# Kernel tuning notes

Measured on AMD Instinct MI355X. Metric: run time of the kernel, lower is better.

The kernel has to match this reference:

```python
import jax, jax.numpy as jnp
import numpy as np

N = 100000
E = 1600000
EPS = 1e-16
NEG_SLOPE = 0.2


def setup_inputs() -> dict:
    key = jax.random.key(0)
    ks = jax.random.split(key, 10)
    F_in, C = 512, 40
    H1, D1 = 8, 8
    return {
        "x": jax.random.normal(ks[0], (N, F_in), jnp.float32),
        "edge_index": jax.random.randint(ks[1], (2, E), 0, N, jnp.int64),
        "W1": jax.random.normal(ks[2], (F_in, H1 * D1), jnp.float32) * 0.05,
        "att_src1": jax.random.normal(ks[3], (H1, D1), jnp.float32) * 0.1,
        "att_dst1": jax.random.normal(ks[4], (H1, D1), jnp.float32) * 0.1,
        "b1": jnp.zeros((H1 * D1,), jnp.float32),
        "W2": jax.random.normal(ks[5], (H1 * D1, C), jnp.float32) * 0.05,
        "att_src2": jax.random.normal(ks[6], (1, C), jnp.float32) * 0.1,
        "att_dst2": jax.random.normal(ks[7], (1, C), jnp.float32) * 0.1,
        "b2": jnp.zeros((C,), jnp.float32),
    }


def gat_conv(x, W, att_src, att_dst, bias, src, dst, heads, out_dim, concat):
    # Linear transform per head: [N, H, D]
    h = (x @ W).reshape(N, heads, out_dim)
    # Per-node attention logits: [N, H]
    a_src = jnp.einsum("nhd,hd->nh", h, att_src)
    a_dst = jnp.einsum("nhd,hd->nh", h, att_dst)
    # Per-edge logits (edge j->i: src=j, softmax grouped by dst=i)
    e = a_src[src] + a_dst[dst]                      # [E', H]
    e = jax.nn.leaky_relu(e, NEG_SLOPE)
    # Segment softmax over destination nodes (numerically stable)
    m = jax.ops.segment_max(e, dst, num_segments=N)  # [N, H]
    e = jnp.exp(e - m[dst])
    s = jax.ops.segment_sum(e, dst, num_segments=N)  # [N, H]
    alpha = e / (s[dst] + EPS)                       # [E', H]
    # Weighted message aggregation (scatter-add)
    msg = h[src] * alpha[:, :, None]                 # [E', H, D]
    out = jax.ops.segment_sum(msg, dst, num_segments=N)  # [N, H, D]
    out = out.reshape(N, heads * out_dim) if concat else out.mean(axis=1)
    return out + bias


def reference(x, edge_index, W1, att_src1, att_dst1, b1, W2, att_src2, att_dst2, b2):
    # PyG GATConv default: add self-loops
    loops = jnp.arange(N, dtype=edge_index.dtype)
    src = jnp.concatenate([edge_index[0], loops])
    dst = jnp.concatenate([edge_index[1], loops])
    h = gat_conv(x, W1, att_src1, att_dst1, b1, src, dst, heads=8, out_dim=8, concat=True)
    h = jax.nn.elu(h)
    out = gat_conv(h, W2, att_src2, att_dst2, b2, src, dst, heads=1, out_dim=40, concat=False)
    return jax.nn.log_softmax(out, axis=1)
```

## Files before the change

kernel.cpp:

```cpp
#include <hip/hip_runtime.h>
#include <cstdint>

#define N_NODES 100000
#define N_EDGES 1600000
#define ETOT    1700000
#define FIN     512
#define HD1     64
#define NB      80
#define C2      40
#define NEG_SLOPE 0.2f
#define SCAN_NB ((N_NODES + 1023) / 1024)

typedef __attribute__((ext_vector_type(8))) short bf16x8;
typedef __attribute__((ext_vector_type(4))) float f32x4;

__device__ __forceinline__ float lrelu(float v) { return v > 0.f ? v : NEG_SLOPE * v; }

__device__ __forceinline__ unsigned short f2bf(float f) {
    uint32_t u = __float_as_uint(f);
    u += 0x7FFF + ((u >> 16) & 1);
    return (unsigned short)(u >> 16);
}
__device__ __forceinline__ float bf2f(unsigned short u) {
    return __uint_as_float(((uint32_t)u) << 16);
}

__global__ void k_prep(const float* __restrict__ W1, const float* __restrict__ a_s,
                       const float* __restrict__ a_d,
                       const float* __restrict__ W2, const float* __restrict__ att_s2,
                       const float* __restrict__ att_d2,
                       unsigned short* __restrict__ W1t, unsigned short* __restrict__ W2t) {
    if (blockIdx.x < 160) {
        int t = blockIdx.x * 256 + threadIdx.x;
        int n = t >> 9, k = t & 511;
        float v;
        if (n < 64) {
            v = W1[k * HD1 + n];
        } else if (n < 72) {
            int h = n - 64; v = 0.f;
#pragma unroll
            for (int d = 0; d < 8; d++) v += W1[k * HD1 + h * 8 + d] * a_s[h * 8 + d];
        } else {
            int h = n - 72; v = 0.f;
#pragma unroll
            for (int d = 0; d < 8; d++) v += W1[k * HD1 + h * 8 + d] * a_d[h * 8 + d];
        }
        W1t[n * FIN + k] = f2bf(v);
    } else {
        int t = (blockIdx.x - 160) * 256 + threadIdx.x;
        if (t >= 48 * 64) return;
        int n = t >> 6, k = t & 63;
        float v = 0.f;
        if (n < C2) {
            v = W2[k * C2 + n];
        } else if (n == C2) {
            for (int c = 0; c < C2; c++) v += W2[k * C2 + c] * att_s2[c];
        } else if (n == C2 + 1) {
            for (int c = 0; c < C2; c++) v += W2[k * C2 + c] * att_d2[c];
        }
        W2t[n * 64 + k] = f2bf(v);
    }
}

__global__ __launch_bounds__(256) void k_gemm1(const float* __restrict__ x,
                                               const unsigned short* __restrict__ W1t,
                                               unsigned short* __restrict__ h1b,
                                               float* __restrict__ as1,
                                               float* __restrict__ ad1) {
    __shared__ unsigned short As[128 * 72];
    const int t    = threadIdx.x;
    const int lane = t & 63, wv = t >> 6;
    const int quad = lane >> 4, l16 = lane & 15;
    const int row0 = blockIdx.x * 128;

    f32x4 acc[2][5];
#pragma unroll
    for (int mi = 0; mi < 2; mi++)
#pragma unroll
        for (int ni = 0; ni < 5; ni++) acc[mi][ni] = (f32x4){0.f, 0.f, 0.f, 0.f};

    float4 rx[8];
#pragma unroll
    for (int i = 0; i < 8; i++) {
        int ff = t + i * 256;
        int r = ff >> 4, c4 = ff & 15;
        int row = row0 + r;
        rx[i] = (row < N_NODES) ? *(const float4*)&x[(size_t)row * FIN + c4 * 4]
                                : make_float4(0.f, 0.f, 0.f, 0.f);
    }

    for (int c = 0; c < 8; c++) {
#pragma unroll
        for (int i = 0; i < 8; i++) {
            int ff = t + i * 256;
            int r = ff >> 4, c4 = ff & 15;
            ushort4 s4;
            s4.x = f2bf(rx[i].x); s4.y = f2bf(rx[i].y);
            s4.z = f2bf(rx[i].z); s4.w = f2bf(rx[i].w);
            *(ushort4*)&As[r * 72 + c4 * 4] = s4;
        }
        __syncthreads();
        if (c < 7) {
            int kb = (c + 1) * 64;
#pragma unroll
            for (int i = 0; i < 8; i++) {
                int ff = t + i * 256;
                int r = ff >> 4, c4 = ff & 15;
                int row = row0 + r;
                rx[i] = (row < N_NODES) ? *(const float4*)&x[(size_t)row * FIN + kb + c4 * 4]
                                        : make_float4(0.f, 0.f, 0.f, 0.f);
            }
        }
        int kb = c * 64;
#pragma unroll
        for (int ks = 0; ks < 2; ks++) {
            bf16x8 af[2], bfv[5];
#pragma unroll
            for (int mi = 0; mi < 2; mi++) {
                int lr = wv * 32 + mi * 16 + l16;
                af[mi] = *(const bf16x8*)&As[lr * 72 + ks * 32 + quad * 8];
            }
#pragma unroll
            for (int ni = 0; ni < 5; ni++) {
                int n = ni * 16 + l16;
                bfv[ni] = *(const bf16x8*)&W1t[n * FIN + kb + ks * 32 + quad * 8];
            }
#pragma unroll
            for (int mi = 0; mi < 2; mi++)
#pragma unroll
                for (int ni = 0; ni < 5; ni++)
                    acc[mi][ni] = __builtin_amdgcn_mfma_f32_16x16x32_bf16(
                        af[mi], bfv[ni], acc[mi][ni], 0, 0, 0);
        }
        __syncthreads();
    }
#pragma unroll
    for (int mi = 0; mi < 2; mi++)
#pragma unroll
        for (int ni = 0; ni < 5; ni++)
#pragma unroll
            for (int r = 0; r < 4; r++) {
                int row = row0 + wv * 32 + mi * 16 + quad * 4 + r;
                if (row >= N_NODES) continue;
                int col = ni * 16 + l16;
                float v = acc[mi][ni][r];
                if (col < 64)       h1b[(size_t)row * 64 + col] = f2bf(v);
                else if (col < 72)  as1[row * 8 + (col - 64)] = v;
                else                ad1[row * 8 + (col - 72)] = v;
            }
}

__global__ void k_deg(const int* __restrict__ ei, int* __restrict__ deg) {
    int e = blockIdx.x * 256 + threadIdx.x;
    if (e >= ETOT) return;
    int dst = (e < N_EDGES) ? ei[N_EDGES + e] : e - N_EDGES;
    atomicAdd(&deg[dst], 1);
}

__global__ __launch_bounds__(1024) void k_bsum(const int* __restrict__ deg,
                                               int* __restrict__ bsum) {
    __shared__ int wsm[16];
    int t = threadIdx.x;
    int i = blockIdx.x * 1024 + t;
    int v = (i < N_NODES) ? deg[i] : 0;
#pragma unroll
    for (int o = 32; o >= 1; o >>= 1) v += __shfl_xor(v, o, 64);
    if ((t & 63) == 0) wsm[t >> 6] = v;
    __syncthreads();
    if (t < 16) {
        int s = wsm[t];
#pragma unroll
        for (int o = 8; o >= 1; o >>= 1) s += __shfl_xor(s, o, 16);
        if (t == 0) bsum[blockIdx.x] = s;
    }
}

__global__ __launch_bounds__(128) void k_bscan(const int* __restrict__ bsum,
                                               int* __restrict__ boff) {
    __shared__ int sh[128];
    int t = threadIdx.x;
    int v = (t < SCAN_NB) ? bsum[t] : 0;
    sh[t] = v;
    __syncthreads();
    for (int off = 1; off < 128; off <<= 1) {
        int u = (t >= off) ? sh[t - off] : 0;
        __syncthreads();
        sh[t] += u;
        __syncthreads();
    }
    boff[t] = sh[t] - v;
}

__global__ __launch_bounds__(1024) void k_scan3(const int* __restrict__ deg,
                                                const int* __restrict__ boff,
                                                int* __restrict__ row_ptr) {
    __shared__ int sh[1024];
    int t = threadIdx.x;
    int i = blockIdx.x * 1024 + t;
    int v = (i < N_NODES) ? deg[i] : 0;
    sh[t] = v;
    __syncthreads();
    for (int off = 1; off < 1024; off <<= 1) {
        int u = (t >= off) ? sh[t - off] : 0;
        __syncthreads();
        sh[t] += u;
        __syncthreads();
    }
    int base = boff[blockIdx.x];
    if (i < N_NODES) row_ptr[i] = base + sh[t] - v;
    if (i == N_NODES - 1) row_ptr[N_NODES] = base + sh[t];
}

__global__ void k_scatter(const int* __restrict__ ei, const int* __restrict__ row_ptr,
                          int* __restrict__ cnt, int* __restrict__ csr_src) {
    int e = blockIdx.x * 256 + threadIdx.x;
    if (e >= ETOT) return;
    int src, dst;
    if (e < N_EDGES) { src = ei[e]; dst = ei[N_EDGES + e]; }
    else             { src = dst = e - N_EDGES; }
    int pos = row_ptr[dst] + atomicAdd(&cnt[dst], 1);
    csr_src[pos] = src;
}

__global__ __launch_bounds__(256) void k_agg1(
    const unsigned short* __restrict__ h1b,
    const float* __restrict__ as1, const float* __restrict__ ad1,
    const int* __restrict__ row_ptr, const int* __restrict__ csr_src,
    const float* __restrict__ b1, unsigned short* __restrict__ hb) {
    int t = threadIdx.x, wv = t >> 6, lane = t & 63;
    int dst = blockIdx.x * 4 + wv;
    if (dst >= N_NODES) return;
    int h = lane >> 3;
    int s0 = row_ptr[dst], s1e = row_ptr[dst + 1];
    float adh = ad1[dst * 8 + h];
    float acc = 0.f, den = 0.f;
    for (int base = s0; base < s1e; base += 64) {
        int idx = base + lane;
        int sl = (idx < s1e) ? csr_src[idx] : 0;
        int cnt = min(64, s1e - base);
        int j = 0;
        for (; j + 4 <= cnt; j += 4) {
#pragma unroll
            for (int jj = 0; jj < 4; jj++) {
                int s = __shfl(sl, j + jj);
                float w = __expf(lrelu(as1[s * 8 + h] + adh));
                den += w;
                acc += w * bf2f(h1b[(size_t)s * 64 + lane]);
            }
        }
        for (; j < cnt; j++) {
            int s = __shfl(sl, j);
            float w = __expf(lrelu(as1[s * 8 + h] + adh));
            den += w;
            acc += w * bf2f(h1b[(size_t)s * 64 + lane]);
        }
    }
    float hv = acc / (den + 1e-16f) + b1[lane];
    hv = hv > 0.f ? hv : expm1f(hv);
    hb[(size_t)dst * 64 + lane] = f2bf(hv);
}

__global__ __launch_bounds__(256) void k_gemm2(const unsigned short* __restrict__ hb,
                                               const unsigned short* __restrict__ W2t,
                                               unsigned short* __restrict__ h2b,
                                               float* __restrict__ as2,
                                               float* __restrict__ ad2) {
    const int t = threadIdx.x;
    const int lane = t & 63, wv = t >> 6;
    const int quad = lane >> 4, l16 = lane & 15;
    const int row0 = blockIdx.x * 128;

    f32x4 acc[2][3];
#pragma unroll
    for (int mi = 0; mi < 2; mi++)
#pragma unroll
        for (int ni = 0; ni < 3; ni++) acc[mi][ni] = (f32x4){0.f, 0.f, 0.f, 0.f};

    bf16x8 bfrag[2][3];
#pragma unroll
    for (int ks = 0; ks < 2; ks++)
#pragma unroll
        for (int ni = 0; ni < 3; ni++)
            bfrag[ks][ni] = *(const bf16x8*)&W2t[(ni * 16 + l16) * 64 + ks * 32 + quad * 8];

#pragma unroll
    for (int mi = 0; mi < 2; mi++) {
        int row = row0 + wv * 32 + mi * 16 + l16;
        int rowc = row < N_NODES ? row : N_NODES - 1;
#pragma unroll
        for (int ks = 0; ks < 2; ks++) {
            bf16x8 af = *(const bf16x8*)&hb[(size_t)rowc * 64 + ks * 32 + quad * 8];
#pragma unroll
            for (int ni = 0; ni < 3; ni++)
                acc[mi][ni] = __builtin_amdgcn_mfma_f32_16x16x32_bf16(
                    af, bfrag[ks][ni], acc[mi][ni], 0, 0, 0);
        }
    }
#pragma unroll
    for (int mi = 0; mi < 2; mi++)
#pragma unroll
        for (int ni = 0; ni < 3; ni++)
#pragma unroll
            for (int r = 0; r < 4; r++) {
                int row = row0 + wv * 32 + mi * 16 + quad * 4 + r;
                if (row >= N_NODES) continue;
                int col = ni * 16 + l16;
                float v = acc[mi][ni][r];
                if (col < C2)            h2b[(size_t)row * C2 + col] = f2bf(v);
                else if (col == C2)      as2[row] = v;
                else if (col == C2 + 1)  ad2[row] = v;
            }
}

__global__ __launch_bounds__(256) void k_agg2(
    const unsigned short* __restrict__ h2b,
    const float* __restrict__ as2, const float* __restrict__ ad2,
    const int* __restrict__ row_ptr, const int* __restrict__ csr_src,
    const float* __restrict__ b2, float* __restrict__ out) {
    int t = threadIdx.x, wv = t >> 6, lane = t & 63;
    int dst = blockIdx.x * 4 + wv;
    if (dst >= N_NODES) return;
    int s0 = row_ptr[dst], s1e = row_ptr[dst + 1];
    float ad = ad2[dst];
    bool act = lane < C2;
    int cl = act ? lane : 0;
    float acc = 0.f, den = 0.f;
    for (int base = s0; base < s1e; base += 64) {
        int idx = base + lane;
        bool vld = idx < s1e;
        int sl = vld ? csr_src[idx] : 0;
        float wl = vld ? __expf(lrelu(as2[sl] + ad)) : 0.f;
        float d = wl;
#pragma unroll
        for (int o = 32; o >= 1; o >>= 1) d += __shfl_xor(d, o, 64);
        den += d;
        int cnt  = min(64, s1e - base);
        int cnt4 = (cnt + 3) & ~3;
        for (int j = 0; j < cnt4; j += 4) {
#pragma unroll
            for (int jj = 0; jj < 4; jj++) {
                int s   = __shfl(sl, j + jj);
                float w = __shfl(wl, j + jj);
                float hvv = bf2f(h2b[(size_t)s * C2 + cl]);
                if (act) acc += w * hvv;
            }
        }
    }
    float v = act ? acc / (den + 1e-16f) + b2[cl] : -1e30f;
    float m = v;
#pragma unroll
    for (int o = 32; o >= 1; o >>= 1) m = fmaxf(m, __shfl_xor(m, o, 64));
    float ex = act ? __expf(v - m) : 0.f;
    float ssum = ex;
#pragma unroll
    for (int o = 32; o >= 1; o >>= 1) ssum += __shfl_xor(ssum, o, 64);
    if (act) out[(size_t)dst * C2 + lane] = v - m - logf(ssum);
}

extern "C" void kernel_launch(void* const* d_in, const int* in_sizes, int n_in,
                              void* d_out, int out_size, void* d_ws, size_t ws_size,
                              hipStream_t stream) {
    const float* x     = (const float*)d_in[0];
    const int*   ei    = (const int*)d_in[1];
    const float* W1    = (const float*)d_in[2];
    const float* at_s1 = (const float*)d_in[3];
    const float* at_d1 = (const float*)d_in[4];
    const float* b1    = (const float*)d_in[5];
    const float* W2    = (const float*)d_in[6];
    const float* at_s2 = (const float*)d_in[7];
    const float* at_d2 = (const float*)d_in[8];
    const float* b2    = (const float*)d_in[9];
    float* out = (float*)d_out;
    float* ws  = (float*)d_ws;

    unsigned short* h1b = (unsigned short*)ws;
    float* as1 = ws + 3200000;
    float* ad1 = ws + 4000000;
    unsigned short* hb  = (unsigned short*)(ws + 4800000);
    unsigned short* h2b = (unsigned short*)(ws + 8000000);
    float* as2 = ws + 10000000;
    float* ad2 = ws + 10100000;
    unsigned short* W1t = (unsigned short*)(ws + 10200000);
    unsigned short* W2t = (unsigned short*)(ws + 10250000);
    int* row_ptr = (int*)(ws + 10300000);
    int* deg     = (int*)(ws + 10410000);
    int* cnt     = (int*)(ws + 10520000);
    int* csr_src = (int*)(ws + 10630000);
    int* bsum    = (int*)(ws + 12340000);
    int* boff    = (int*)(ws + 12350000);

    hipMemsetAsync(deg, 0, (size_t)N_NODES * sizeof(int), stream);
    hipMemsetAsync(cnt, 0, (size_t)N_NODES * sizeof(int), stream);

    k_prep<<<172, 256, 0, stream>>>(W1, at_s1, at_d1, W2, at_s2, at_d2, W1t, W2t);
    k_deg<<<(ETOT + 255) / 256, 256, 0, stream>>>(ei, deg);
    k_bsum<<<SCAN_NB, 1024, 0, stream>>>(deg, bsum);
    k_bscan<<<1, 128, 0, stream>>>(bsum, boff);
    k_scan3<<<SCAN_NB, 1024, 0, stream>>>(deg, boff, row_ptr);
    k_scatter<<<(ETOT + 255) / 256, 256, 0, stream>>>(ei, row_ptr, cnt, csr_src);
    k_gemm1<<<(N_NODES + 127) / 128, 256, 0, stream>>>(x, W1t, h1b, as1, ad1);
    k_agg1<<<(N_NODES + 3) / 4, 256, 0, stream>>>(h1b, as1, ad1, row_ptr, csr_src, b1, hb);
    k_gemm2<<<(N_NODES + 127) / 128, 256, 0, stream>>>(hb, W2t, h2b, as2, ad2);
    k_agg2<<<(N_NODES + 3) / 4, 256, 0, stream>>>(h2b, as2, ad2, row_ptr, csr_src, b2, out);
}
```

Baseline: 616.8 us.

## Vectorize edge aggregation across 8-lane groups and reuse degree atomic for CSR slots

Aggregation kernels now assign one edge per 8-lane group with 16-byte bf16 row loads, processing 8 edges per wave iteration and reducing across groups with shuffles. The CSR build records each edge's atomic slot during degree counting, so the scatter needs no second atomic pass. The degree memset is folded into the prep kernel and the count buffer is dropped. It needs extra workspace for the slot array and adds a cross-group shuffle reduction.

```diff
diff --git a/kernel.cpp b/kernel.cpp
--- a/kernel.cpp
+++ b/kernel.cpp
@@ -6,7 +6,6 @@
 #define ETOT    1700000
 #define FIN     512
 #define HD1     64
-#define NB      80
 #define C2      40
 #define NEG_SLOPE 0.2f
 #define SCAN_NB ((N_NODES + 1023) / 1024)
@@ -29,10 +28,12 @@
                        const float* __restrict__ a_d,
                        const float* __restrict__ W2, const float* __restrict__ att_s2,
                        const float* __restrict__ att_d2,
-                       unsigned short* __restrict__ W1t, unsigned short* __restrict__ W2t) {
-    if (blockIdx.x < 160) {
-        int t = blockIdx.x * 256 + threadIdx.x;
-        int n = t >> 9, k = t & 511;
+                       unsigned short* __restrict__ W1t, unsigned short* __restrict__ W2t,
+                       int* __restrict__ deg) {
+    int i = blockIdx.x * 256 + threadIdx.x;
+    if (i < N_NODES) deg[i] = 0;
+    if (i < 80 * 512) {
+        int n = i >> 9, k = i & 511;
         float v;
         if (n < 64) {
             v = W1[k * HD1 + n];
@@ -46,10 +47,9 @@
             for (int d = 0; d < 8; d++) v += W1[k * HD1 + h * 8 + d] * a_d[h * 8 + d];
         }
         W1t[n * FIN + k] = f2bf(v);
-    } else {
-        int t = (blockIdx.x - 160) * 256 + threadIdx.x;
-        if (t >= 48 * 64) return;
-        int n = t >> 6, k = t & 63;
+    } else if (i < 80 * 512 + 48 * 64) {
+        int j = i - 80 * 512;
+        int n = j >> 6, k = j & 63;
         float v = 0.f;
         if (n < C2) {
             v = W2[k * C2 + n];
@@ -150,11 +150,12 @@
             }
 }
 
-__global__ void k_deg(const int* __restrict__ ei, int* __restrict__ deg) {
+__global__ void k_degord(const int* __restrict__ ei, int* __restrict__ deg,
+                         int* __restrict__ ord) {
     int e = blockIdx.x * 256 + threadIdx.x;
     if (e >= ETOT) return;
     int dst = (e < N_EDGES) ? ei[N_EDGES + e] : e - N_EDGES;
-    atomicAdd(&deg[dst], 1);
+    ord[e] = atomicAdd(&deg[dst], 1);
 }
 
 __global__ __launch_bounds__(1024) void k_bsum(const int* __restrict__ deg,
@@ -212,14 +213,13 @@
 }
 
 __global__ void k_scatter(const int* __restrict__ ei, const int* __restrict__ row_ptr,
-                          int* __restrict__ cnt, int* __restrict__ csr_src) {
+                          const int* __restrict__ ord, int* __restrict__ csr_src) {
     int e = blockIdx.x * 256 + threadIdx.x;
     if (e >= ETOT) return;
     int src, dst;
     if (e < N_EDGES) { src = ei[e]; dst = ei[N_EDGES + e]; }
     else             { src = dst = e - N_EDGES; }
-    int pos = row_ptr[dst] + atomicAdd(&cnt[dst], 1);
-    csr_src[pos] = src;
+    csr_src[row_ptr[dst] + ord[e]] = src;
 }
 
 __global__ __launch_bounds__(256) void k_agg1(
@@ -230,34 +230,47 @@
     int t = threadIdx.x, wv = t >> 6, lane = t & 63;
     int dst = blockIdx.x * 4 + wv;
     if (dst >= N_NODES) return;
-    int h = lane >> 3;
+    int g = lane >> 3, i8 = lane & 7;
     int s0 = row_ptr[dst], s1e = row_ptr[dst + 1];
-    float adh = ad1[dst * 8 + h];
-    float acc = 0.f, den = 0.f;
+    float adh = ad1[dst * 8 + i8];
+    float den = 0.f;
+    float facc[8];
+#pragma unroll
+    for (int d = 0; d < 8; d++) facc[d] = 0.f;
+
     for (int base = s0; base < s1e; base += 64) {
         int idx = base + lane;
         int sl = (idx < s1e) ? csr_src[idx] : 0;
         int cnt = min(64, s1e - base);
-        int j = 0;
-        for (; j + 4 <= cnt; j += 4) {
-#pragma unroll
-            for (int jj = 0; jj < 4; jj++) {
-                int s = __shfl(sl, j + jj);
-                float w = __expf(lrelu(as1[s * 8 + h] + adh));
-                den += w;
-                acc += w * bf2f(h1b[(size_t)s * 64 + lane]);
-            }
-        }
-        for (; j < cnt; j++) {
-            int s = __shfl(sl, j);
-            float w = __expf(lrelu(as1[s * 8 + h] + adh));
+        for (int j = 0; j < cnt; j += 8) {
+            int s = __shfl(sl, j + g);
+            bool vld = (j + g) < cnt;
+            float w = vld ? __expf(lrelu(as1[s * 8 + i8] + adh)) : 0.f;
             den += w;
-            acc += w * bf2f(h1b[(size_t)s * 64 + lane]);
-        }
-    }
-    float hv = acc / (den + 1e-16f) + b1[lane];
-    hv = hv > 0.f ? hv : expm1f(hv);
-    hb[(size_t)dst * 64 + lane] = f2bf(hv);
+            bf16x8 hrow = *(const bf16x8*)&h1b[(size_t)s * 64 + i8 * 8];
+#pragma unroll
+            for (int d = 0; d < 8; d++)
+                facc[d] += w * bf2f((unsigned short)hrow[d]);
+        }
+    }
+#pragma unroll
+    for (int o = 8; o <= 32; o <<= 1) {
+        den += __shfl_xor(den, o, 64);
+#pragma unroll
+        for (int d = 0; d < 8; d++) facc[d] += __shfl_xor(facc[d], o, 64);
+    }
+    float rden = 1.f / (den + 1e-16f);
+    float4 b1lo = *(const float4*)&b1[i8 * 8];
+    float4 b1hi = *(const float4*)&b1[i8 * 8 + 4];
+    float bb[8] = {b1lo.x, b1lo.y, b1lo.z, b1lo.w, b1hi.x, b1hi.y, b1hi.z, b1hi.w};
+    bf16x8 pk;
+#pragma unroll
+    for (int d = 0; d < 8; d++) {
+        float hv = facc[d] * rden + bb[d];
+        hv = hv > 0.f ? hv : expm1f(hv);
+        pk[d] = (short)f2bf(hv);
+    }
+    if (g == 0) *(bf16x8*)&hb[(size_t)dst * 64 + i8 * 8] = pk;
 }
 
 __global__ __launch_bounds__(256) void k_gemm2(const unsigned short* __restrict__ hb,
@@ -320,41 +333,62 @@
     int t = threadIdx.x, wv = t >> 6, lane = t & 63;
     int dst = blockIdx.x * 4 + wv;
     if (dst >= N_NODES) return;
+    int g = lane >> 3, i8 = lane & 7;
+    bool act = i8 < 5;
+    int off = act ? i8 * 8 : 0;
     int s0 = row_ptr[dst], s1e = row_ptr[dst + 1];
     float ad = ad2[dst];
-    bool act = lane < C2;
-    int cl = act ? lane : 0;
-    float acc = 0.f, den = 0.f;
+    float denp = 0.f;
+    float facc[8];
+#pragma unroll
+    for (int d = 0; d < 8; d++) facc[d] = 0.f;
+
     for (int base = s0; base < s1e; base += 64) {
         int idx = base + lane;
-        bool vld = idx < s1e;
-        int sl = vld ? csr_src[idx] : 0;
-        float wl = vld ? __expf(lrelu(as2[sl] + ad)) : 0.f;
-        float d = wl;
-#pragma unroll
-        for (int o = 32; o >= 1; o >>= 1) d += __shfl_xor(d, o, 64);
-        den += d;
-        int cnt  = min(64, s1e - base);
-        int cnt4 = (cnt + 3) & ~3;
-        for (int j = 0; j < cnt4; j += 4) {
-#pragma unroll
-            for (int jj = 0; jj < 4; jj++) {
-                int s   = __shfl(sl, j + jj);
-                float w = __shfl(wl, j + jj);
-                float hvv = bf2f(h2b[(size_t)s * C2 + cl]);
-                if (act) acc += w * hvv;
-            }
-        }
-    }
-    float v = act ? acc / (den + 1e-16f) + b2[cl] : -1e30f;
-    float m = v;
-#pragma unroll
-    for (int o = 32; o >= 1; o >>= 1) m = fmaxf(m, __shfl_xor(m, o, 64));
-    float ex = act ? __expf(v - m) : 0.f;
-    float ssum = ex;
-#pragma unroll
-    for (int o = 32; o >= 1; o >>= 1) ssum += __shfl_xor(ssum, o, 64);
-    if (act) out[(size_t)dst * C2 + lane] = v - m - logf(ssum);
+        int sl = (idx < s1e) ? csr_src[idx] : 0;
+        int cnt = min(64, s1e - base);
+        for (int j = 0; j < cnt; j += 8) {
+            int s = __shfl(sl, j + g);
+            bool vld = (j + g) < cnt;
+            float wf = vld ? __expf(lrelu(as2[s] + ad)) : 0.f;
+            if (i8 == 0) denp += wf;
+            float w = act ? wf : 0.f;
+            bf16x8 hrow = *(const bf16x8*)&h2b[(size_t)s * C2 + off];
+#pragma unroll
+            for (int d = 0; d < 8; d++)
+                facc[d] += w * bf2f((unsigned short)hrow[d]);
+        }
+    }
+#pragma unroll
+    for (int o = 8; o <= 32; o <<= 1)
+#pragma unroll
+        for (int d = 0; d < 8; d++) facc[d] += __shfl_xor(facc[d], o, 64);
+    float den = denp;
+#pragma unroll
+    for (int o = 32; o >= 1; o >>= 1) den += __shfl_xor(den, o, 64);
+    float rden = 1.f / (den + 1e-16f);
+
+    float vch[8];
+    float mx = -1e30f;
+#pragma unroll
+    for (int d = 0; d < 8; d++) {
+        vch[d] = act ? facc[d] * rden + b2[off + d] : -1e30f;
+        mx = fmaxf(mx, vch[d]);
+    }
+#pragma unroll
+    for (int o = 1; o <= 4; o <<= 1) mx = fmaxf(mx, __shfl_xor(mx, o, 64));
+    float es = 0.f;
+#pragma unroll
+    for (int d = 0; d < 8; d++) es += act ? __expf(vch[d] - mx) : 0.f;
+#pragma unroll
+    for (int o = 1; o <= 4; o <<= 1) es += __shfl_xor(es, o, 64);
+    float lg = logf(es);
+    if (g == 0 && act) {
+        float4 o0 = {vch[0] - mx - lg, vch[1] - mx - lg, vch[2] - mx - lg, vch[3] - mx - lg};
+        float4 o1 = {vch[4] - mx - lg, vch[5] - mx - lg, vch[6] - mx - lg, vch[7] - mx - lg};
+        *(float4*)&out[(size_t)dst * C2 + i8 * 8]     = o0;
+        *(float4*)&out[(size_t)dst * C2 + i8 * 8 + 4] = o1;
+    }
 }
 
 extern "C" void kernel_launch(void* const* d_in, const int* in_sizes, int n_in,
@@ -384,20 +418,17 @@
     unsigned short* W2t = (unsigned short*)(ws + 10250000);
     int* row_ptr = (int*)(ws + 10300000);
     int* deg     = (int*)(ws + 10410000);
-    int* cnt     = (int*)(ws + 10520000);
     int* csr_src = (int*)(ws + 10630000);
     int* bsum    = (int*)(ws + 12340000);
     int* boff    = (int*)(ws + 12350000);
-
-    hipMemsetAsync(deg, 0, (size_t)N_NODES * sizeof(int), stream);
-    hipMemsetAsync(cnt, 0, (size_t)N_NODES * sizeof(int), stream);
-
-    k_prep<<<172, 256, 0, stream>>>(W1, at_s1, at_d1, W2, at_s2, at_d2, W1t, W2t);
-    k_deg<<<(ETOT + 255) / 256, 256, 0, stream>>>(ei, deg);
+    int* ord     = (int*)(ws + 13000000);
+
+    k_prep<<<391, 256, 0, stream>>>(W1, at_s1, at_d1, W2, at_s2, at_d2, W1t, W2t, deg);
+    k_degord<<<(ETOT + 255) / 256, 256, 0, stream>>>(ei, deg, ord);
     k_bsum<<<SCAN_NB, 1024, 0, stream>>>(deg, bsum);
     k_bscan<<<1, 128, 0, stream>>>(bsum, boff);
     k_scan3<<<SCAN_NB, 1024, 0, stream>>>(deg, boff, row_ptr);
-    k_scatter<<<(ETOT + 255) / 256, 256, 0, stream>>>(ei, row_ptr, cnt, csr_src);
+    k_scatter<<<(ETOT + 255) / 256, 256, 0, stream>>>(ei, row_ptr, ord, csr_src);
     k_gemm1<<<(N_NODES + 127) / 128, 256, 0, stream>>>(x, W1t, h1b, as1, ad1);
     k_agg1<<<(N_NODES + 3) / 4, 256, 0, stream>>>(h1b, as1, ad1, row_ptr, csr_src, b1, hb);
     k_gemm2<<<(N_NODES + 127) / 128, 256, 0, stream>>>(hb, W2t, h2b, as2, ad2);
```

Result: faster. 593.6 us (-3.8%).
